# Kernel optimization log

Measured on AMD Instinct MI355X. Metric: run time of the kernel, lower is better.

The kernel has to match this reference:

```python
import jax, jax.numpy as jnp
from jax import lax
import numpy as np


def setup_inputs() -> dict:
    key = jax.random.key(0)
    ks = jax.random.split(key, 9)
    B, L, Dm = 2, 2048, 768
    di, ds, dc = 1536, 16, 4
    def w(k, shape, fan_in):
        return jax.random.normal(k, shape, jnp.float32) / np.sqrt(fan_in)
    return {
        "x": jax.random.normal(ks[0], (B, L, Dm), jnp.float32),
        "W_in": w(ks[1], (2 * di, Dm), Dm),
        "W_conv": w(ks[2], (di, 1, dc), dc),          # depthwise conv kernel (torch layout)
        "W_x": w(ks[3], (2 * ds, di), di),
        "W_dt": w(ks[4], (di, di), di),
        "b_dt": jax.random.normal(ks[5], (di,), jnp.float32) * 0.1,
        "A_log": jnp.log(jnp.arange(1, ds + 1, dtype=jnp.float32)),
        "D": jnp.ones((di,), jnp.float32),
        "W_out": w(ks[6], (Dm, di), di),
    }


def reference(x, W_in, W_conv, W_x, W_dt, b_dt, A_log, D, W_out):
    B, L, Dm = x.shape
    di = W_in.shape[0] // 2
    ds = A_log.shape[0]
    dc = W_conv.shape[-1]

    xz = x @ W_in.T                                   # (B,L,2*di)
    x_part, z = xz[..., :di], xz[..., di:]

    # causal depthwise conv1d (torch pads dc-1 both sides then truncates -> left pad only)
    xc = lax.conv_general_dilated(
        x_part.transpose(0, 2, 1), W_conv, window_strides=(1,),
        padding=[(dc - 1, 0)], feature_group_count=di)  # (B,di,L)
    xc = jax.nn.silu(xc.transpose(0, 2, 1))            # (B,L,di)

    A = -jnp.exp(A_log)                                # (ds,)
    x_dbl = xc @ W_x.T                                 # (B,L,2*ds)
    B_ssm, C_ssm = x_dbl[..., :ds], x_dbl[..., ds:]
    delta = jax.nn.softplus(xc @ W_dt.T + b_dt)        # (B,L,di)

    deltaA = jnp.exp(delta[..., None] * A)             # (B,L,di,ds)
    deltaB = delta[..., None] * B_ssm[:, :, None, :]   # (B,L,di,ds)

    def step(h, inp):
        dA_t, dB_t, C_t = inp                          # (B,di,ds),(B,di,ds),(B,ds)
        h = dA_t * h + dB_t
        y = jnp.einsum('bds,bs->bd', h, C_t)
        return h, y

    h0 = jnp.zeros((B, di, ds), x.dtype)
    _, ys = lax.scan(step, h0, (deltaA.transpose(1, 0, 2, 3),
                                deltaB.transpose(1, 0, 2, 3),
                                C_ssm.transpose(1, 0, 2)))
    y = ys.transpose(1, 0, 2) + D * xc                 # (B,L,di)
    y = y * jax.nn.silu(z)
    return y @ W_out.T                                 # (B,L,Dm)
```

## Files before the change

kernel.cpp:

```cpp
#include <hip/hip_runtime.h>
#include <hip/hip_bf16.h>

#define BB 2
#define LL 2048
#define DM 768
#define DI 1536
#define DS 16
#define MM (BB*LL)
#define NCH 64
#define CHL 32
#define SEQS (BB*DI*DS)
#define NC2 1664

typedef __hip_bfloat16 bf16;
typedef short bf16x8 __attribute__((ext_vector_type(8)));
typedef float f32x4  __attribute__((ext_vector_type(4)));

__device__ __forceinline__ void gl_lds16(const void* g, void* l) {
  __builtin_amdgcn_global_load_lds((const __attribute__((address_space(1))) void*)g,
                                   (__attribute__((address_space(3))) void*)l, 16, 0, 0);
}

__device__ __forceinline__ bf16x8 ds_frag(const short* lds) {
  bf16x8 r;
  unsigned off = (unsigned)(uintptr_t)(const __attribute__((address_space(3))) short*)lds;
  asm volatile("ds_read_b128 %0, %1" : "=v"(r) : "v"(off));
  return r;
}

struct bf4 { __hip_bfloat16 a, b, c, d; };
#define PR0 786432
#define PR1 589824
#define PR2 294912
#define PR3 638976
#define PRTOT (PR0+PR1+PR2+PR3)

__global__ __launch_bounds__(256) void prep_k(const float* __restrict__ x,
                                              const float* __restrict__ Win,
                                              const float* __restrict__ Wout,
                                              const float* __restrict__ Wdt,
                                              const float* __restrict__ Wx,
                                              __hip_bfloat16* __restrict__ xbf,
                                              __hip_bfloat16* __restrict__ Winbf,
                                              __hip_bfloat16* __restrict__ Woutbf,
                                              __hip_bfloat16* __restrict__ Wcomb) {
  int i = blockIdx.x * 256 + threadIdx.x;
  if (i >= PRTOT) return;
  float4 v; __hip_bfloat16* dst; int di_;
  if (i < PR0)                    { v = ((const float4*)x)[i];                 dst = xbf;    di_ = i; }
  else if (i < PR0 + PR1)         { di_ = i - PR0; v = ((const float4*)Win)[di_];  dst = Winbf; }
  else if (i < PR0 + PR1 + PR2)   { di_ = i - PR0 - PR1; v = ((const float4*)Wout)[di_]; dst = Woutbf; }
  else {
    di_ = i - PR0 - PR1 - PR2;
    int e = di_ * 4, row = e / DI, colb = e % DI;
    if (row < DI)            v = ((const float4*)Wdt)[di_];
    else if (row < DI + 32)  v = *(const float4*)(Wx + (size_t)(row - DI) * DI + colb);
    else                     v = make_float4(0.f, 0.f, 0.f, 0.f);
    dst = Wcomb;
  }
  bf4 o = { __float2bfloat16(v.x), __float2bfloat16(v.y),
            __float2bfloat16(v.z), __float2bfloat16(v.w) };
  ((bf4*)dst)[di_] = o;
}

template<int EPI, int BM>
__global__ __launch_bounds__(256) void gemm_db(const bf16* __restrict__ A,
                                               const bf16* __restrict__ W,
                                               void* __restrict__ Cv,
                                               void* __restrict__ C2v,
                                               const float* __restrict__ bias,
                                               int M, int N, int K, int Kstride) {
  constexpr int NA  = BM / 64;
  constexpr int LPT = NA + 2;
  __shared__ short sA[4][BM * 32];
  __shared__ short sB[4][128 * 32];
  const int t = threadIdx.x;

  const int gx = gridDim.x, gy = gridDim.y;
  const int n3 = gx * gy * gridDim.z;
  const int hw = blockIdx.x + gx * (blockIdx.y + gy * blockIdx.z);
  const int per = n3 >> 3;
  const int wl  = (hw & 7) * per + (hw >> 3);
  const int wz  = wl / (gx * gy);
  const int rem = wl - wz * (gx * gy);
  const int wy  = rem / gx, wx = rem - wy * gx;

  const int m0 = wy * BM, n0 = wx * 128;
  const size_t koff = (size_t)wz * K;
  const int w = t >> 6, lane = t & 63;
  const int wm = (w >> 1) * (BM / 2), wn = (w & 1) * 64;
  const int ga = wm >> 4, gb = wn >> 4;

  f32x4 acc[BM / 32][4] = {};

  const int srow = lane & 15, skoff = (lane >> 4) * 8;
  const bf16* gA[NA]; const bf16* gB[2];
  #pragma unroll
  for (int j = 0; j < NA; j++)
    gA[j] = A + (size_t)(m0 + (w + 4 * j) * 16 + srow) * Kstride + koff + skoff;
  #pragma unroll
  for (int j = 0; j < 2; j++)
    gB[j] = W + (size_t)(n0 + (w + 4 * j) * 16 + srow) * Kstride + koff + skoff;

  #define ISSUE(buf, k0)                                              \
    do {                                                              \
      _Pragma("unroll")                                               \
      for (int j = 0; j < NA; j++)                                    \
        gl_lds16(gA[j] + (k0), &sA[buf][(w + 4 * j) * 512]);          \
      _Pragma("unroll")                                               \
      for (int j = 0; j < 2; j++)                                     \
        gl_lds16(gB[j] + (k0), &sB[buf][(w + 4 * j) * 512]);          \
    } while (0)

  ISSUE(0, 0);
  ISSUE(1, 32);
  ISSUE(2, 64);
  int p = 0;
  for (int k0 = 0; k0 < K; k0 += 32) {
    if (k0 + 64 < K) {
      asm volatile("s_waitcnt vmcnt(%0)" :: "n"(2 * LPT));
    } else if (k0 + 32 < K) {
      asm volatile("s_waitcnt vmcnt(%0)" :: "n"(LPT));
    } else {
      asm volatile("s_waitcnt vmcnt(0)");
    }
    __builtin_amdgcn_s_barrier();
    if (k0 + 96 < K) {
      int nb = p + 3; if (nb >= 4) nb -= 4;
      ISSUE(nb, k0 + 96);
    }
    const short* baseA = sA[p];
    const short* baseB = sB[p];
    bf16x8 af[BM / 32], bfr[4];
    #pragma unroll
    for (int i = 0; i < BM / 32; i++) af[i]  = ds_frag(baseA + ((ga + i) * 64 + lane) * 8);
    #pragma unroll
    for (int j = 0; j < 4; j++)       bfr[j] = ds_frag(baseB + ((gb + j) * 64 + lane) * 8);
    asm volatile("s_waitcnt lgkmcnt(0)");
    __builtin_amdgcn_sched_barrier(0);
    #pragma unroll
    for (int i = 0; i < BM / 32; i++)
      #pragma unroll
      for (int j = 0; j < 4; j++)
        acc[i][j] = __builtin_amdgcn_mfma_f32_16x16x32_bf16(af[i], bfr[j], acc[i][j], 0, 0, 0);
    p++; if (p >= 4) p = 0;
  }
  #undef ISSUE

  const int q = lane >> 4, mm = lane & 15;
  #pragma unroll
  for (int i = 0; i < BM / 32; i++)
    #pragma unroll
    for (int j = 0; j < 4; j++) {
      int r0  = m0 + wm + i * 16 + q * 4;
      int col = n0 + wn + j * 16 + mm;
      #pragma unroll
      for (int r = 0; r < 4; r++) {
        float v = acc[i][j][r];
        if (EPI == 5) {
          if (col < DI) ((bf16*)Cv) [(size_t)(r0 + r) * DI + col]        = __float2bfloat16(v);
          else          ((bf16*)C2v)[(size_t)(r0 + r) * DI + (col - DI)] = __float2bfloat16(v);
        } else if (EPI == 6) {
          if (col < DI) {
            float vv = v + bias[col];
            vv = (vv > 15.f) ? vv : __logf(1.f + __expf(vv));
            ((bf16*)Cv)[(size_t)(r0 + r) * DI + col] = __float2bfloat16(vv);
          } else if (col < DI + 32) {
            ((float*)C2v)[(size_t)(r0 + r) * 32 + (col - DI)] = v;
          }
        } else {
          ((float*)Cv)[(size_t)wz * M * N + (size_t)(r0 + r) * N + col] = v;
        }
      }
    }
}

__global__ __launch_bounds__(256) void redk_k(const float4* __restrict__ P,
                                              float4* __restrict__ out, int n4) {
  int i = blockIdx.x * 256 + threadIdx.x;
  if (i >= n4) return;
  float4 a = P[i], b = P[i + n4];
  out[i] = make_float4(a.x + b.x, a.y + b.y, a.z + b.z, a.w + b.w);
}

__global__ __launch_bounds__(256) void conv_silu_k(const bf16* __restrict__ xpart,
                                                   const float* __restrict__ Wc,
                                                   __hip_bfloat16* __restrict__ xcbf) {
  int idx = blockIdx.x * 256 + threadIdx.x;
  if (idx >= MM * DI) return;
  int d = idx % DI;
  int r = idx / DI;
  int l = r & (LL - 1);
  float4 wv = ((const float4*)Wc)[d];
  const bf16* xp = xpart + (size_t)r * DI + d;
  float acc = wv.w * __bfloat162float(xp[0]);
  if (l >= 1) acc += wv.z * __bfloat162float(xp[-(ptrdiff_t)DI]);
  if (l >= 2) acc += wv.y * __bfloat162float(xp[-(ptrdiff_t)(2 * DI)]);
  if (l >= 3) acc += wv.x * __bfloat162float(xp[-(ptrdiff_t)(3 * DI)]);
  float s = acc / (1.f + __expf(-acc));
  xcbf[idx] = __float2bfloat16(s);
}

__global__ __launch_bounds__(64) void scan_part_k(const bf16* __restrict__ delta,
                                                  const float* __restrict__ xdbl,
                                                  const float* __restrict__ A_log,
                                                  float* __restrict__ prodA,
                                                  float* __restrict__ hend) {
  __shared__ float sBC[CHL * 32];
  const int t = threadIdx.x;
  const int dg = blockIdx.x % (DI / 64);
  const int chunk = (blockIdx.x / (DI / 64)) % NCH;
  const int b = blockIdx.x / ((DI / 64) * NCH);
  const int d = dg * 64 + t;

  float a[16];
  #pragma unroll
  for (int s = 0; s < 16; s++) a[s] = -__expf(A_log[s]);

  const float4* src = (const float4*)(xdbl + ((size_t)b * LL + chunk * CHL) * 32);
  #pragma unroll
  for (int k = 0; k < CHL * 32 / 4 / 64; k++) ((float4*)sBC)[t + k * 64] = src[t + k * 64];
  __syncthreads();

  float h[16], p[16];
  #pragma unroll
  for (int s = 0; s < 16; s++) { h[s] = 0.f; p[s] = 1.f; }

  const bf16* dptr = delta + ((size_t)b * LL + chunk * CHL) * DI + d;
  #pragma unroll 2
  for (int i = 0; i < CHL; i++) {
    float dlt = __bfloat162float(dptr[(size_t)i * DI]);
    const float4* bc = (const float4*)(sBC + i * 32);
    float4 B0 = bc[0], B1 = bc[1], B2 = bc[2], B3 = bc[3];
    float Bv[16] = {B0.x,B0.y,B0.z,B0.w, B1.x,B1.y,B1.z,B1.w,
                    B2.x,B2.y,B2.z,B2.w, B3.x,B3.y,B3.z,B3.w};
    #pragma unroll
    for (int s = 0; s < 16; s++) {
      float dA = __expf(dlt * a[s]);
      h[s] = dA * h[s] + dlt * Bv[s];
      p[s] *= dA;
    }
  }
  size_t o = (size_t)chunk * SEQS + ((size_t)b * DI + d) * 16;
  #pragma unroll
  for (int s = 0; s < 16; s += 4) {
    ((float4*)(prodA + o))[s >> 2] = make_float4(p[s], p[s+1], p[s+2], p[s+3]);
    ((float4*)(hend  + o))[s >> 2] = make_float4(h[s], h[s+1], h[s+2], h[s+3]);
  }
}

__global__ __launch_bounds__(64) void scan_comb_k(const float* __restrict__ prodA,
                                                  const float* __restrict__ hend,
                                                  float* __restrict__ hstart) {
  int idx = blockIdx.x * 64 + threadIdx.x;
  float run = 0.f;
  #pragma unroll 4
  for (int c = 0; c < NCH; c++) {
    size_t o = (size_t)c * SEQS + idx;
    hstart[o] = run;
    run = prodA[o] * run + hend[o];
  }
}

__global__ __launch_bounds__(64) void scan_fin_k(const bf16* __restrict__ delta,
                                                 const float* __restrict__ xdbl,
                                                 const float* __restrict__ A_log,
                                                 const float* __restrict__ Dp,
                                                 const bf16* __restrict__ xcbf,
                                                 const bf16* __restrict__ zbf,
                                                 const float* __restrict__ hstart,
                                                 __hip_bfloat16* __restrict__ ypbf) {
  __shared__ float sBC[CHL * 32];
  const int t = threadIdx.x;
  const int dg = blockIdx.x % (DI / 64);
  const int chunk = (blockIdx.x / (DI / 64)) % NCH;
  const int b = blockIdx.x / ((DI / 64) * NCH);
  const int d = dg * 64 + t;

  float a[16];
  #pragma unroll
  for (int s = 0; s < 16; s++) a[s] = -__expf(A_log[s]);

  const float4* src = (const float4*)(xdbl + ((size_t)b * LL + chunk * CHL) * 32);
  #pragma unroll
  for (int k = 0; k < CHL * 32 / 4 / 64; k++) ((float4*)sBC)[t + k * 64] = src[t + k * 64];
  __syncthreads();

  float h[16];
  size_t o = (size_t)chunk * SEQS + ((size_t)b * DI + d) * 16;
  #pragma unroll
  for (int s = 0; s < 16; s += 4) {
    float4 v = ((const float4*)(hstart + o))[s >> 2];
    h[s] = v.x; h[s+1] = v.y; h[s+2] = v.z; h[s+3] = v.w;
  }
  const float Dv = Dp[d];

  const size_t rbase = (size_t)b * LL + chunk * CHL;
  const bf16* dptr = delta + rbase * DI + d;
  const bf16* xcp  = xcbf  + rbase * DI + d;
  const bf16* zp   = zbf   + rbase * DI + d;
  __hip_bfloat16* yp = ypbf + rbase * DI + d;

  #pragma unroll 2
  for (int i = 0; i < CHL; i++) {
    float dlt = __bfloat162float(dptr[(size_t)i * DI]);
    const float4* bc = (const float4*)(sBC + i * 32);
    float4 B0 = bc[0], B1 = bc[1], B2 = bc[2], B3 = bc[3];
    float4 C0 = bc[4], C1 = bc[5], C2 = bc[6], C3 = bc[7];
    float Bv[16] = {B0.x,B0.y,B0.z,B0.w, B1.x,B1.y,B1.z,B1.w,
                    B2.x,B2.y,B2.z,B2.w, B3.x,B3.y,B3.z,B3.w};
    float Cv[16] = {C0.x,C0.y,C0.z,C0.w, C1.x,C1.y,C1.z,C1.w,
                    C2.x,C2.y,C2.z,C2.w, C3.x,C3.y,C3.z,C3.w};
    float y = 0.f;
    #pragma unroll
    for (int s = 0; s < 16; s++) {
      float dA = __expf(dlt * a[s]);
      h[s] = dA * h[s] + dlt * Bv[s];
      y += h[s] * Cv[s];
    }
    float xcv = __bfloat162float(xcp[(size_t)i * DI]);
    float zv  = __bfloat162float(zp [(size_t)i * DI]);
    float val = (y + Dv * xcv) * (zv / (1.f + __expf(-zv)));
    yp[(size_t)i * DI] = __float2bfloat16(val);
  }
}

extern "C" void kernel_launch(void* const* d_in, const int* in_sizes, int n_in,
                              void* d_out, int out_size, void* d_ws, size_t ws_size,
                              hipStream_t stream) {
  const float* x      = (const float*)d_in[0];
  const float* W_in   = (const float*)d_in[1];
  const float* W_conv = (const float*)d_in[2];
  const float* W_x    = (const float*)d_in[3];
  const float* W_dt   = (const float*)d_in[4];
  const float* b_dt   = (const float*)d_in[5];
  const float* A_log  = (const float*)d_in[6];
  const float* Dp     = (const float*)d_in[7];
  const float* W_out  = (const float*)d_in[8];
  float* out = (float*)d_out;

  char* ws = (char*)d_ws;
  bf16*  xpartbf = (bf16*)(ws + 0);
  bf16*  zbf     = (bf16*)(ws + 12582912);
  bf16*  xbf     = (bf16*)(ws + 25165824);
  bf16*  Winbf   = (bf16*)(ws + 31457280);
  bf16*  xcbf    = (bf16*)(ws + 36175872);
  bf16*  Wcomb   = (bf16*)(ws + 48758784);
  bf16*  deltabf = (bf16*)(ws + 53870592);
  float* xdbl    = (float*)(ws + 66453504);
  bf16*  ypbf    = (bf16*)(ws + 66977792);
  bf16*  Woutbf  = (bf16*)(ws + 79560704);
  float* prodA   = (float*)(ws + 81920000);
  float* hend    = (float*)(ws + 94502912);
  float* hstart  = (float*)(ws + 107085824);
  float* P3      = (float*)(ws + 0);

  prep_k<<<(PRTOT + 255) / 256, 256, 0, stream>>>(x, W_in, W_out, W_dt, W_x,
                                                  xbf, Winbf, Woutbf, Wcomb);

  {
    dim3 g(3072 / 128, 4096 / 128, 1);
    gemm_db<5, 128><<<g, 256, 0, stream>>>(xbf, Winbf, xpartbf, zbf, nullptr,
                                           MM, 2 * DI, DM, DM);
  }
  conv_silu_k<<<(MM * DI + 255) / 256, 256, 0, stream>>>(xpartbf, W_conv, xcbf);
  {
    dim3 g(NC2 / 128, 4096 / 128, 1);
    gemm_db<6, 128><<<g, 256, 0, stream>>>(xcbf, Wcomb, deltabf, xdbl, b_dt,
                                           MM, NC2, DI, DI);
  }
  scan_part_k<<<BB * NCH * (DI / 64), 64, 0, stream>>>(deltabf, xdbl, A_log, prodA, hend);
  scan_comb_k<<<SEQS / 64, 64, 0, stream>>>(prodA, hend, hstart);
  scan_fin_k<<<BB * NCH * (DI / 64), 64, 0, stream>>>(deltabf, xdbl, A_log, Dp, xcbf, zbf,
                                                      hstart, ypbf);
  {
    dim3 g(768 / 128, 4096 / 128, 2);
    gemm_db<7, 128><<<g, 256, 0, stream>>>(ypbf, Woutbf, P3, nullptr, nullptr,
                                           MM, DM, DI / 2, DI);
  }
  redk_k<<<(786432 + 255) / 256, 256, 0, stream>>>((const float4*)P3, (float4*)out, 786432);
}
```

Before: 329.8 us.

## Restructure GEMM main loop to process two K-steps per barrier with paired buffers

The GEMM main loop now consumes two 32-wide K slices per iteration from a pair of LDS buffers. It loads fragments for both slices up front and runs the first slice's MFMAs while the second slice's LDS reads finish. Refills for the next pair are issued only after a second barrier, so buffers are overwritten strictly after use. The intent is to halve per-K-step wait and barrier overhead and to overlap LDS reads with MFMA work. The vmcnt and lgkmcnt wait counts are hardcoded to 8, which only matches the BM=128 instantiation, and K must be a multiple of 64.

```diff
diff --git a/kernel.cpp b/kernel.cpp
--- a/kernel.cpp
+++ b/kernel.cpp
@@ -71,7 +71,6 @@
                                                const float* __restrict__ bias,
                                                int M, int N, int K, int Kstride) {
   constexpr int NA  = BM / 64;
-  constexpr int LPT = NA + 2;
   __shared__ short sA[4][BM * 32];
   __shared__ short sB[4][128 * 32];
   const int t = threadIdx.x;
@@ -112,38 +111,52 @@
         gl_lds16(gB[j] + (k0), &sB[buf][(w + 4 * j) * 512]);          \
     } while (0)
 
-  ISSUE(0, 0);
-  ISSUE(1, 32);
-  ISSUE(2, 64);
-  int p = 0;
-  for (int k0 = 0; k0 < K; k0 += 32) {
-    if (k0 + 64 < K) {
-      asm volatile("s_waitcnt vmcnt(%0)" :: "n"(2 * LPT));
-    } else if (k0 + 32 < K) {
-      asm volatile("s_waitcnt vmcnt(%0)" :: "n"(LPT));
+  ISSUE(0, 0);  ISSUE(1, 32);
+  ISSUE(2, 64); ISSUE(3, 96);
+
+  const int NI = K >> 6;
+  for (int i = 0; i < NI; ++i) {
+    if (i + 1 < NI) {
+      asm volatile("s_waitcnt vmcnt(%0)" :: "n"(8));
     } else {
       asm volatile("s_waitcnt vmcnt(0)");
     }
     __builtin_amdgcn_s_barrier();
-    if (k0 + 96 < K) {
-      int nb = p + 3; if (nb >= 4) nb -= 4;
-      ISSUE(nb, k0 + 96);
-    }
-    const short* baseA = sA[p];
-    const short* baseB = sB[p];
-    bf16x8 af[BM / 32], bfr[4];
-    #pragma unroll
-    for (int i = 0; i < BM / 32; i++) af[i]  = ds_frag(baseA + ((ga + i) * 64 + lane) * 8);
-    #pragma unroll
-    for (int j = 0; j < 4; j++)       bfr[j] = ds_frag(baseB + ((gb + j) * 64 + lane) * 8);
+
+    const int pb = (i & 1) << 1;
+    const short* bA0 = sA[pb];     const short* bB0 = sB[pb];
+    const short* bA1 = sA[pb + 1]; const short* bB1 = sB[pb + 1];
+
+    bf16x8 afA[BM / 32], bfA[4], afB[BM / 32], bfB[4];
+    #pragma unroll
+    for (int q2 = 0; q2 < BM / 32; q2++) afA[q2] = ds_frag(bA0 + ((ga + q2) * 64 + lane) * 8);
+    #pragma unroll
+    for (int j = 0; j < 4; j++)          bfA[j]  = ds_frag(bB0 + ((gb + j) * 64 + lane) * 8);
+    #pragma unroll
+    for (int q2 = 0; q2 < BM / 32; q2++) afB[q2] = ds_frag(bA1 + ((ga + q2) * 64 + lane) * 8);
+    #pragma unroll
+    for (int j = 0; j < 4; j++)          bfB[j]  = ds_frag(bB1 + ((gb + j) * 64 + lane) * 8);
+
+    asm volatile("s_waitcnt lgkmcnt(%0)" :: "n"(8));
+    __builtin_amdgcn_sched_barrier(0);
+    #pragma unroll
+    for (int q2 = 0; q2 < BM / 32; q2++)
+      #pragma unroll
+      for (int j = 0; j < 4; j++)
+        acc[q2][j] = __builtin_amdgcn_mfma_f32_16x16x32_bf16(afA[q2], bfA[j], acc[q2][j], 0, 0, 0);
+
     asm volatile("s_waitcnt lgkmcnt(0)");
     __builtin_amdgcn_sched_barrier(0);
-    #pragma unroll
-    for (int i = 0; i < BM / 32; i++)
+    __builtin_amdgcn_s_barrier();
+    if (i + 2 < NI) {
+      const int kn = (i + 2) << 6;
+      ISSUE(pb, kn); ISSUE(pb + 1, kn + 32);
+    }
+    #pragma unroll
+    for (int q2 = 0; q2 < BM / 32; q2++)
       #pragma unroll
       for (int j = 0; j < 4; j++)
-        acc[i][j] = __builtin_amdgcn_mfma_f32_16x16x32_bf16(af[i], bfr[j], acc[i][j], 0, 0, 0);
-    p++; if (p >= 4) p = 0;
+        acc[q2][j] = __builtin_amdgcn_mfma_f32_16x16x32_bf16(afB[q2], bfB[j], acc[q2][j], 0, 0, 0);
   }
   #undef ISSUE
 
```

Measured after the change: 333.2 us. Within noise of the previous version (+1.0%).

## Replace LDS-staged GEMM pipeline with direct-to-register triple-buffered loads

Applied to the files above, without the earlier changes.

Removes the shared-memory staging (global_load_lds plus ds_read fragments and barriers) from the bf16 MFMA GEMM. Each wave now loads its MFMA fragments straight from global memory into registers and rotates three register buffers to prefetch ahead. This drops the LDS traffic and the block-level barriers. In exchange, tiles shared between waves are no longer reused, so global/L2 traffic doubles, register pressure rises, and the loads are narrower and less coalesced. It also relies on K being a multiple of 96, which holds for all three call sites (768, 1536, 768).

```diff
diff --git a/kernel.cpp b/kernel.cpp
--- a/kernel.cpp
+++ b/kernel.cpp
@@ -15,18 +15,6 @@
 typedef __hip_bfloat16 bf16;
 typedef short bf16x8 __attribute__((ext_vector_type(8)));
 typedef float f32x4  __attribute__((ext_vector_type(4)));
-
-__device__ __forceinline__ void gl_lds16(const void* g, void* l) {
-  __builtin_amdgcn_global_load_lds((const __attribute__((address_space(1))) void*)g,
-                                   (__attribute__((address_space(3))) void*)l, 16, 0, 0);
-}
-
-__device__ __forceinline__ bf16x8 ds_frag(const short* lds) {
-  bf16x8 r;
-  unsigned off = (unsigned)(uintptr_t)(const __attribute__((address_space(3))) short*)lds;
-  asm volatile("ds_read_b128 %0, %1" : "=v"(r) : "v"(off));
-  return r;
-}
 
 struct bf4 { __hip_bfloat16 a, b, c, d; };
 #define PR0 786432
@@ -64,16 +52,12 @@
 }
 
 template<int EPI, int BM>
-__global__ __launch_bounds__(256) void gemm_db(const bf16* __restrict__ A,
+__global__ __launch_bounds__(256) void gemm_dr(const bf16* __restrict__ A,
                                                const bf16* __restrict__ W,
                                                void* __restrict__ Cv,
                                                void* __restrict__ C2v,
                                                const float* __restrict__ bias,
                                                int M, int N, int K, int Kstride) {
-  constexpr int NA  = BM / 64;
-  constexpr int LPT = NA + 2;
-  __shared__ short sA[4][BM * 32];
-  __shared__ short sB[4][128 * 32];
   const int t = threadIdx.x;
 
   const int gx = gridDim.x, gy = gridDim.y;
@@ -89,63 +73,50 @@
   const size_t koff = (size_t)wz * K;
   const int w = t >> 6, lane = t & 63;
   const int wm = (w >> 1) * (BM / 2), wn = (w & 1) * 64;
-  const int ga = wm >> 4, gb = wn >> 4;
 
   f32x4 acc[BM / 32][4] = {};
 
   const int srow = lane & 15, skoff = (lane >> 4) * 8;
-  const bf16* gA[NA]; const bf16* gB[2];
-  #pragma unroll
-  for (int j = 0; j < NA; j++)
-    gA[j] = A + (size_t)(m0 + (w + 4 * j) * 16 + srow) * Kstride + koff + skoff;
-  #pragma unroll
-  for (int j = 0; j < 2; j++)
-    gB[j] = W + (size_t)(n0 + (w + 4 * j) * 16 + srow) * Kstride + koff + skoff;
-
-  #define ISSUE(buf, k0)                                              \
-    do {                                                              \
-      _Pragma("unroll")                                               \
-      for (int j = 0; j < NA; j++)                                    \
-        gl_lds16(gA[j] + (k0), &sA[buf][(w + 4 * j) * 512]);          \
-      _Pragma("unroll")                                               \
-      for (int j = 0; j < 2; j++)                                     \
-        gl_lds16(gB[j] + (k0), &sB[buf][(w + 4 * j) * 512]);          \
-    } while (0)
-
-  ISSUE(0, 0);
-  ISSUE(1, 32);
-  ISSUE(2, 64);
-  int p = 0;
-  for (int k0 = 0; k0 < K; k0 += 32) {
-    if (k0 + 64 < K) {
-      asm volatile("s_waitcnt vmcnt(%0)" :: "n"(2 * LPT));
-    } else if (k0 + 32 < K) {
-      asm volatile("s_waitcnt vmcnt(%0)" :: "n"(LPT));
-    } else {
-      asm volatile("s_waitcnt vmcnt(0)");
-    }
-    __builtin_amdgcn_s_barrier();
-    if (k0 + 96 < K) {
-      int nb = p + 3; if (nb >= 4) nb -= 4;
-      ISSUE(nb, k0 + 96);
-    }
-    const short* baseA = sA[p];
-    const short* baseB = sB[p];
-    bf16x8 af[BM / 32], bfr[4];
-    #pragma unroll
-    for (int i = 0; i < BM / 32; i++) af[i]  = ds_frag(baseA + ((ga + i) * 64 + lane) * 8);
-    #pragma unroll
-    for (int j = 0; j < 4; j++)       bfr[j] = ds_frag(baseB + ((gb + j) * 64 + lane) * 8);
-    asm volatile("s_waitcnt lgkmcnt(0)");
-    __builtin_amdgcn_sched_barrier(0);
-    #pragma unroll
-    for (int i = 0; i < BM / 32; i++)
-      #pragma unroll
-      for (int j = 0; j < 4; j++)
-        acc[i][j] = __builtin_amdgcn_mfma_f32_16x16x32_bf16(af[i], bfr[j], acc[i][j], 0, 0, 0);
-    p++; if (p >= 4) p = 0;
-  }
-  #undef ISSUE
+  const bf16* pa[BM / 32]; const bf16* pb[4];
+  #pragma unroll
+  for (int i = 0; i < BM / 32; i++)
+    pa[i] = A + (size_t)(m0 + wm + i * 16 + srow) * Kstride + koff + skoff;
+  #pragma unroll
+  for (int j = 0; j < 4; j++)
+    pb[j] = W + (size_t)(n0 + wn + j * 16 + srow) * Kstride + koff + skoff;
+
+  bf16x8 Xa[BM / 32], Xb[4], Ya[BM / 32], Yb[4], Za[BM / 32], Zb[4];
+
+#define LDB(Ba, Bb, kk)                                                       \
+  do {                                                                        \
+    _Pragma("unroll")                                                         \
+    for (int i_ = 0; i_ < BM / 32; i_++)                                      \
+      Ba[i_] = *(const bf16x8*)(pa[i_] + (kk));                               \
+    _Pragma("unroll")                                                         \
+    for (int j_ = 0; j_ < 4; j_++)                                            \
+      Bb[j_] = *(const bf16x8*)(pb[j_] + (kk));                               \
+  } while (0)
+
+#define CMP(Ba, Bb)                                                           \
+  do {                                                                        \
+    _Pragma("unroll")                                                         \
+    for (int i_ = 0; i_ < BM / 32; i_++)                                      \
+      _Pragma("unroll")                                                       \
+      for (int j_ = 0; j_ < 4; j_++)                                          \
+        acc[i_][j_] = __builtin_amdgcn_mfma_f32_16x16x32_bf16(                \
+            Ba[i_], Bb[j_], acc[i_][j_], 0, 0, 0);                            \
+  } while (0)
+
+  LDB(Xa, Xb, 0);
+  LDB(Ya, Yb, 32);
+  LDB(Za, Zb, 64);
+  for (int k0 = 0; k0 < K; k0 += 96) {
+    CMP(Xa, Xb); if (k0 + 96  < K) LDB(Xa, Xb, k0 + 96);
+    CMP(Ya, Yb); if (k0 + 128 < K) LDB(Ya, Yb, k0 + 128);
+    CMP(Za, Zb); if (k0 + 160 < K) LDB(Za, Zb, k0 + 160);
+  }
+#undef LDB
+#undef CMP
 
   const int q = lane >> 4, mm = lane & 15;
   #pragma unroll
@@ -360,13 +331,13 @@
 
   {
     dim3 g(3072 / 128, 4096 / 128, 1);
-    gemm_db<5, 128><<<g, 256, 0, stream>>>(xbf, Winbf, xpartbf, zbf, nullptr,
+    gemm_dr<5, 128><<<g, 256, 0, stream>>>(xbf, Winbf, xpartbf, zbf, nullptr,
                                            MM, 2 * DI, DM, DM);
   }
   conv_silu_k<<<(MM * DI + 255) / 256, 256, 0, stream>>>(xpartbf, W_conv, xcbf);
   {
     dim3 g(NC2 / 128, 4096 / 128, 1);
-    gemm_db<6, 128><<<g, 256, 0, stream>>>(xcbf, Wcomb, deltabf, xdbl, b_dt,
+    gemm_dr<6, 128><<<g, 256, 0, stream>>>(xcbf, Wcomb, deltabf, xdbl, b_dt,
                                            MM, NC2, DI, DI);
   }
   scan_part_k<<<BB * NCH * (DI / 64), 64, 0, stream>>>(deltabf, xdbl, A_log, prodA, hend);
@@ -375,7 +346,7 @@
                                                       hstart, ypbf);
   {
     dim3 g(768 / 128, 4096 / 128, 2);
-    gemm_db<7, 128><<<g, 256, 0, stream>>>(ypbf, Woutbf, P3, nullptr, nullptr,
+    gemm_dr<7, 128><<<g, 256, 0, stream>>>(ypbf, Woutbf, P3, nullptr, nullptr,
                                            MM, DM, DI / 2, DI);
   }
   redk_k<<<(786432 + 255) / 256, 256, 0, stream>>>((const float4*)P3, (float4*)out, 786432);
```

New measurement: 421.4 us. +27.8%, slower.
